# Optimization experiments

Measured on AMD Instinct MI355X. Metric: run time of the kernel, lower is better.

The kernel has to match this reference:

```python
import jax, jax.numpy as jnp
import numpy as np

N_NODES = 50000
N_EDGES = 800000
HIDDEN = 64
RES = 0.5  # args.res_layer


def setup_inputs() -> dict:
    key = jax.random.key(0)
    ks = jax.random.split(key, 9)
    s = 0.05  # scale weights to keep exp(att) stable
    return {
        "edge_index": jax.random.randint(ks[0], (2, N_EDGES), 0, N_NODES, dtype=jnp.int32),
        "adj_values": jax.random.uniform(ks[1], (N_EDGES,), dtype=jnp.float32),
        "embeds": jax.random.normal(ks[2], (N_NODES, HIDDEN), dtype=jnp.float32),
        "W1": jax.random.normal(ks[3], (HIDDEN, HIDDEN), dtype=jnp.float32) * s,
        "b1": jax.random.normal(ks[4], (HIDDEN,), dtype=jnp.float32) * s,
        "W2": jax.random.normal(ks[5], (HIDDEN, HIDDEN), dtype=jnp.float32) * s,
        "b2": jax.random.normal(ks[6], (HIDDEN,), dtype=jnp.float32) * s,
        "att_w": jax.random.normal(ks[7], (2 * HIDDEN,), dtype=jnp.float32) * s,
        "att_b": jax.random.normal(ks[8], (1,), dtype=jnp.float32) * s,
    }


def reference(edge_index, adj_values, embeds, W1, b1, W2, b2, att_w, att_b):
    n = embeds.shape[0]
    h = embeds.shape[1]
    row, col = edge_index[0], edge_index[1]
    # per-edge gather + two small linears with ReLU
    f1 = jax.nn.relu(embeds[row] @ W1 + b1)          # [E, h]
    f2 = jax.nn.relu(embeds[col] @ W2 + b2)          # [E, h]
    # attention score = Linear(concat(f1, f2)) -> split weight, avoid concat
    att = f1 @ att_w[:h] + f2 @ att_w[h:] + att_b[0]  # [E]
    exp_att = jnp.exp(att)
    # sparse row-wise softmax denominator via segment sum
    rowsum = jax.ops.segment_sum(exp_att, row, num_segments=n) + 1e-6  # [N]
    values = (exp_att / rowsum[row] + RES * adj_values) / (1.0 + RES)  # [E]
    # SpMM: out[i] = sum_{e: row[e]=i} values[e] * embeds[col[e]]
    out = jax.ops.segment_sum(values[:, None] * embeds[col], row, num_segments=n)  # [N, h]
    return values, out
```

## Files before the change

### kernel.cpp

```cpp
#include <hip/hip_runtime.h>
#include <hip/hip_bf16.h>

#define HID 64
#define RES_F 0.5f
#define NBKT 196
#define BCAP 5120
#define EB   512
#define LCAP 32

typedef __attribute__((ext_vector_type(8))) short short8;
typedef __attribute__((ext_vector_type(4))) float f32x4;

__device__ __forceinline__ short f2bf(float x) {
    __hip_bfloat16 h = __float2bfloat16(x);
    return __builtin_bit_cast(short, h);
}
__device__ __forceinline__ float bf2f(unsigned short u) {
    return __builtin_bit_cast(float, ((unsigned)u) << 16);
}

__global__ void __launch_bounds__(256) fused_prep_kernel(
    const float* __restrict__ embeds,
    const float* __restrict__ W1, const float* __restrict__ W2,
    const float* __restrict__ b1, const float* __restrict__ b2,
    const float* __restrict__ att_w, const float* __restrict__ att_b,
    const int* __restrict__ row, const int* __restrict__ col,
    const float* __restrict__ adj,
    int2* __restrict__ bstream, int* __restrict__ bcnt,
    float* __restrict__ g, float* __restrict__ corr,
    __hip_bfloat16* __restrict__ embeds_bf,
    int n, int E, int nodeBlocks)
{
    __shared__ short sW[2 * HID * HID];

    if (blockIdx.x < nodeBlocks) {
        for (int i = threadIdx.x; i < HID * HID; i += blockDim.x) {
            sW[i]             = f2bf(W1[i]);
            sW[HID * HID + i] = f2bf(W2[i]);
        }
        __syncthreads();

        const float ab = att_b[0];
        const int lane = threadIdx.x & 63;
        const int colx = lane & 15;
        const int quad = lane >> 4;

        short8 bfrag[8][2];
        float  sac[8], bc[8];
#pragma unroll
        for (int cb = 0; cb < 8; ++cb) {
            const int jp = cb * 16 + colx;
            const short* w = (jp < HID) ? (sW + jp) : (sW + HID * HID + jp - HID);
#pragma unroll
            for (int kh = 0; kh < 2; ++kh) {
                short8 f;
#pragma unroll
                for (int j = 0; j < 8; ++j) {
                    const int k = kh * 32 + quad * 8 + j;
                    f[j] = w[k * HID];
                }
                bfrag[cb][kh] = f;
            }
            sac[cb] = att_w[jp];
            bc[cb]  = (jp < HID) ? b1[jp] : b2[jp - HID];
        }

        int gwave = (blockIdx.x * blockDim.x + threadIdx.x) >> 6;
        const int nwave = (nodeBlocks * blockDim.x) >> 6;
        const int nbatch = (n + 15) >> 4;

        for (int b = gwave; b < nbatch; b += nwave) {
            const int base = b << 4;
            int mrow = base + colx;
            if (mrow >= n) mrow = n - 1;
            const float* ep = embeds + (size_t)mrow * HID;
            short8 afrag0, afrag1;
#pragma unroll
            for (int j = 0; j < 8; ++j) {
                afrag0[j] = f2bf(ep[quad * 8 + j]);
                afrag1[j] = f2bf(ep[32 + quad * 8 + j]);
            }
            {
                short8* ebf = (short8*)(embeds_bf + (size_t)mrow * HID);
                ebf[quad]     = afrag0;
                ebf[4 + quad] = afrag1;
            }

            float acc1[4] = {0.f, 0.f, 0.f, 0.f};
            float acc2[4] = {0.f, 0.f, 0.f, 0.f};
#pragma unroll
            for (int cb = 0; cb < 8; ++cb) {
                f32x4 C = {0.f, 0.f, 0.f, 0.f};
                C = __builtin_amdgcn_mfma_f32_16x16x32_bf16(afrag0, bfrag[cb][0], C, 0, 0, 0);
                C = __builtin_amdgcn_mfma_f32_16x16x32_bf16(afrag1, bfrag[cb][1], C, 0, 0, 0);
#pragma unroll
                for (int reg = 0; reg < 4; ++reg) {
                    const float v = fmaxf(C[reg] + bc[cb], 0.f) * sac[cb];
                    if (cb < 4) acc1[reg] += v; else acc2[reg] += v;
                }
            }
#pragma unroll
            for (int reg = 0; reg < 4; ++reg) {
#pragma unroll
                for (int off = 1; off < 16; off <<= 1) {
                    acc1[reg] += __shfl_xor(acc1[reg], off, 64);
                    acc2[reg] += __shfl_xor(acc2[reg], off, 64);
                }
            }
            if (colx == 0) {
#pragma unroll
                for (int reg = 0; reg < 4; ++reg) {
                    const int i = base + quad * 4 + reg;
                    if (i < n) {
                        g[i]    = __expf(acc2[reg]);
                        corr[i] = 1e-6f * __expf(-(acc1[reg] + ab));
                    }
                }
            }
        }
    } else {
        int* lcnt = (int*)sW;
        for (int k = threadIdx.x; k < NBKT; k += 256) lcnt[k] = 0;
        __syncthreads();

        const int eb = blockIdx.x - nodeBlocks;
        const int chunk = (E + EB - 1) / EB;
        const int e0 = eb * chunk;
        const int e1 = min(E, e0 + chunk);
        for (int e = e0 + (int)threadIdx.x; e < e1; e += 256) {
            const int r    = row[e];
            const int c    = col[e];
            const float aj = adj[e];
            const unsigned aq = (unsigned)(aj * 65535.0f + 0.5f);
            const int k = r >> 8;
            const int2 pl = make_int2((int)((unsigned)c | (aq << 16)),
                                      (r & 255) | (e << 8));
            const int pos = atomicAdd(&lcnt[k], 1);
            if (pos < LCAP)
                bstream[((size_t)k * EB + eb) * LCAP + pos] = pl;
        }
        __syncthreads();

        for (int k = threadIdx.x; k < NBKT; k += 256)
            bcnt[eb * NBKT + k] = min(lcnt[k], LCAP);
    }
}

__global__ void __launch_bounds__(512) regroup_kernel(
    const int2* __restrict__ bstream, const int* __restrict__ bcnt,
    int2* __restrict__ edata2, int* __restrict__ rowdir, int n)
{
    __shared__ int cnt[256], wcur[256], wsum[4];
    const int k = blockIdx.x;
    const int t = threadIdx.x;

    if (t < 256) cnt[t] = 0;
    const int myc = bcnt[t * NBKT + k];
    __syncthreads();

    const int2* src = bstream + ((size_t)k * EB + t) * LCAP;
    for (int j = 0; j < myc; ++j)
        atomicAdd(&cnt[src[j].y & 255], 1);
    __syncthreads();

    int incl = 0, myCnt = 0;
    if (t < 256) {
        const int lane = t & 63;
        myCnt = cnt[t];
        incl = myCnt;
#pragma unroll
        for (int off = 1; off < 64; off <<= 1) {
            const int y = __shfl_up(incl, off, 64);
            if (lane >= off) incl += y;
        }
        if (lane == 63) wsum[t >> 6] = incl;
    }
    __syncthreads();
    if (t < 256) {
        int wo = 0;
        for (int i = 0; i < (t >> 6); ++i) wo += wsum[i];
        const int excl = incl + wo - myCnt;
        wcur[t] = excl;
        const int r = k * 256 + t;
        if (r < n)
            rowdir[r] = (k * BCAP + excl) | (min(myCnt, 64) << 20);
    }
    __syncthreads();

    int2* dst = edata2 + (size_t)k * BCAP;
    for (int j = 0; j < myc; ++j) {
        const int2 pl = src[j];
        const int p = atomicAdd(&wcur[pl.y & 255], 1);
        dst[p] = pl;
    }
}

__global__ void __launch_bounds__(256) spmm_kernel(
    const int* __restrict__ rowdir, const int2* __restrict__ edata2,
    const __hip_bfloat16* __restrict__ embeds_bf,
    const float* __restrict__ g, const float* __restrict__ corr,
    float* __restrict__ values, float* __restrict__ out, int n)
{
    const float inv = 1.0f / (1.0f + RES_F);
    const int lane = threadIdx.x & 63;
    const int half = lane >> 5;
    const int hl   = lane & 31;

    const int idx = ((blockIdx.x >> 3) << 2) + (threadIdx.x >> 6);
    const int k   = ((idx >> 8) << 3) + (blockIdx.x & 7);
    const int r   = (k << 8) + (idx & 255);
    if (k >= NBKT || r >= n) return;

    const int pk    = rowdir[r];
    const int start = pk & 0xFFFFF;
    const int deg   = pk >> 20;
    const bool valid = lane < deg;
    int c = 0, e = 0;
    float gc = 0.0f, aj = 0.0f;
    if (valid) {
        const int2 ed = edata2[(size_t)start + lane];
        const unsigned pk0 = (unsigned)ed.x;
        c  = (int)(pk0 & 0xFFFFu);
        aj = (float)(pk0 >> 16) * (1.0f / 65535.0f);
        e  = (int)(((unsigned)ed.y) >> 8);
        gc = g[c];
    }
    float G = gc;
#pragma unroll
    for (int off = 1; off < 64; off <<= 1)
        G += __shfl_xor(G, off, 64);
    const float invDr = 1.0f / (G + corr[r]);
    float v = 0.0f;
    if (valid) {
        v = (gc * invDr + RES_F * aj) * inv;
        values[e] = v;
    }

    float accx = 0.0f, accy = 0.0f;
    int j = 0;
    for (; j + 8 <= deg; j += 8) {
        const int j0 = j + half,     j1 = j + 2 + half;
        const int j2 = j + 4 + half, j3 = j + 6 + half;
        const int   c0 = __shfl(c, j0, 64);
        const int   c1 = __shfl(c, j1, 64);
        const int   c2 = __shfl(c, j2, 64);
        const int   c3 = __shfl(c, j3, 64);
        const float v0 = __shfl(v, j0, 64);
        const float v1 = __shfl(v, j1, 64);
        const float v2 = __shfl(v, j2, 64);
        const float v3 = __shfl(v, j3, 64);
        const ushort2 h0 = *(const ushort2*)(embeds_bf + (size_t)c0 * HID + hl * 2);
        const ushort2 h1 = *(const ushort2*)(embeds_bf + (size_t)c1 * HID + hl * 2);
        const ushort2 h2 = *(const ushort2*)(embeds_bf + (size_t)c2 * HID + hl * 2);
        const ushort2 h3 = *(const ushort2*)(embeds_bf + (size_t)c3 * HID + hl * 2);
        accx = fmaf(v0, bf2f(h0.x), accx); accy = fmaf(v0, bf2f(h0.y), accy);
        accx = fmaf(v1, bf2f(h1.x), accx); accy = fmaf(v1, bf2f(h1.y), accy);
        accx = fmaf(v2, bf2f(h2.x), accx); accy = fmaf(v2, bf2f(h2.y), accy);
        accx = fmaf(v3, bf2f(h3.x), accx); accy = fmaf(v3, bf2f(h3.y), accy);
    }
    for (; j < deg; j += 2) {
        const int j0 = j + half;
        const int   cj = __shfl(c, j0, 64);
        const float vj = __shfl(v, j0, 64);
        const ushort2 h = *(const ushort2*)(embeds_bf + (size_t)cj * HID + hl * 2);
        accx = fmaf(vj, bf2f(h.x), accx);
        accy = fmaf(vj, bf2f(h.y), accy);
    }
    accx += __shfl_xor(accx, 32, 64);
    accy += __shfl_xor(accy, 32, 64);
    if (lane < 32) {
        float2 o; o.x = accx; o.y = accy;
        ((float2*)(out + (size_t)r * HID))[hl] = o;
    }
}

extern "C" void kernel_launch(void* const* d_in, const int* in_sizes, int n_in,
                              void* d_out, int out_size, void* d_ws, size_t ws_size,
                              hipStream_t stream_)
{
    const int* edge_index = (const int*)d_in[0];
    const float* adj      = (const float*)d_in[1];
    const float* embeds   = (const float*)d_in[2];
    const float* W1       = (const float*)d_in[3];
    const float* b1       = (const float*)d_in[4];
    const float* W2       = (const float*)d_in[5];
    const float* b2       = (const float*)d_in[6];
    const float* att_w    = (const float*)d_in[7];
    const float* att_b    = (const float*)d_in[8];

    const int E = in_sizes[1];
    const int N = in_sizes[2] / HID;

    const int* row = edge_index;
    const int* col = edge_index + E;

    int2*  bstream = (int2*)d_ws;
    int2*  edata2  = bstream + (size_t)NBKT * EB * LCAP;
    int*   bcnt    = (int*)(edata2 + (size_t)NBKT * BCAP);
    int*   rowdir  = bcnt + EB * NBKT;
    float* g       = (float*)(rowdir + N);
    float* corr    = g + N;
    __hip_bfloat16* embeds_bf = (__hip_bfloat16*)(corr + N);

    float* values = (float*)d_out;
    float* out    = values + E;

    const int nodeBlocks = 512;
    fused_prep_kernel<<<nodeBlocks + EB, 256, 0, stream_>>>(
        embeds, W1, W2, b1, b2, att_w, att_b, row, col, adj,
        bstream, bcnt, g, corr, embeds_bf,
        N, E, nodeBlocks);

    regroup_kernel<<<NBKT, 512, 0, stream_>>>(bstream, bcnt, edata2, rowdir, N);

    spmm_kernel<<<12800, 256, 0, stream_>>>(rowdir, edata2, embeds_bf,
                                            g, corr, values, out, N);
}
```

Before: 142.7 us.

## Fuse regroup and SpMM into one kernel using LDS-resident bucket edges

Merges the regroup and SpMM kernels. Each bucket is handled by two 1024-thread blocks that redundantly regroup the whole bucket's edges into shared memory and then each process half of its 256 rows. This removes the edata2/rowdir global round trip and one kernel launch. In exchange, the regroup work is done twice per bucket, and only 392 large blocks run the SpMM phase, which may hurt latency hiding for the gathers. The prep kernel also switches the embedding row reads to float4 vector loads.

Result: slower. 154.4 us (+8.3%).

```diff
diff --git a/kernel.cpp b/kernel.cpp
--- a/kernel.cpp
+++ b/kernel.cpp
@@ -73,13 +73,18 @@
             const int base = b << 4;
             int mrow = base + colx;
             if (mrow >= n) mrow = n - 1;
-            const float* ep = embeds + (size_t)mrow * HID;
+            const float4* ep4 = (const float4*)(embeds + (size_t)mrow * HID);
+            const float4 wa = ep4[quad * 2],     wb = ep4[quad * 2 + 1];
+            const float4 wc = ep4[8 + quad * 2], wd = ep4[8 + quad * 2 + 1];
             short8 afrag0, afrag1;
-#pragma unroll
-            for (int j = 0; j < 8; ++j) {
-                afrag0[j] = f2bf(ep[quad * 8 + j]);
-                afrag1[j] = f2bf(ep[32 + quad * 8 + j]);
-            }
+            afrag0[0] = f2bf(wa.x); afrag0[1] = f2bf(wa.y);
+            afrag0[2] = f2bf(wa.z); afrag0[3] = f2bf(wa.w);
+            afrag0[4] = f2bf(wb.x); afrag0[5] = f2bf(wb.y);
+            afrag0[6] = f2bf(wb.z); afrag0[7] = f2bf(wb.w);
+            afrag1[0] = f2bf(wc.x); afrag1[1] = f2bf(wc.y);
+            afrag1[2] = f2bf(wc.z); afrag1[3] = f2bf(wc.w);
+            afrag1[4] = f2bf(wd.x); afrag1[5] = f2bf(wd.y);
+            afrag1[6] = f2bf(wd.z); afrag1[7] = f2bf(wd.w);
             {
                 short8* ebf = (short8*)(embeds_bf + (size_t)mrow * HID);
                 ebf[quad]     = afrag0;
@@ -146,131 +151,130 @@
     }
 }
 
-__global__ void __launch_bounds__(512) regroup_kernel(
+__global__ void __launch_bounds__(1024) regroup_spmm_kernel(
     const int2* __restrict__ bstream, const int* __restrict__ bcnt,
-    int2* __restrict__ edata2, int* __restrict__ rowdir, int n)
+    const __hip_bfloat16* __restrict__ embeds_bf,
+    const float* __restrict__ g, const float* __restrict__ corr,
+    float* __restrict__ values, float* __restrict__ out, int n)
 {
-    __shared__ int cnt[256], wcur[256], wsum[4];
-    const int k = blockIdx.x;
-    const int t = threadIdx.x;
+    __shared__ int2 led[BCAP];
+    __shared__ int cnt[256], rstart[256], wcur[256], wsum[4];
+    const int k   = blockIdx.x >> 1;
+    const int sub = blockIdx.x & 1;
+    const int t   = threadIdx.x;
+    const int sl  = t & 511;
+    const bool hi = t >= 512;
 
     if (t < 256) cnt[t] = 0;
-    const int myc = bcnt[t * NBKT + k];
-    __syncthreads();
-
-    const int2* src = bstream + ((size_t)k * EB + t) * LCAP;
-    for (int j = 0; j < myc; ++j)
+    const int myc = bcnt[sl * NBKT + k];
+    const int jm  = (myc + 1) >> 1;
+    const int j0  = hi ? jm : 0;
+    const int j1  = hi ? myc : jm;
+    __syncthreads();
+
+    const int2* src = bstream + ((size_t)k * EB + sl) * LCAP;
+    for (int j = j0; j < j1; ++j)
         atomicAdd(&cnt[src[j].y & 255], 1);
     __syncthreads();
 
     int incl = 0, myCnt = 0;
     if (t < 256) {
-        const int lane = t & 63;
+        const int lane0 = t & 63;
         myCnt = cnt[t];
         incl = myCnt;
 #pragma unroll
         for (int off = 1; off < 64; off <<= 1) {
             const int y = __shfl_up(incl, off, 64);
-            if (lane >= off) incl += y;
-        }
-        if (lane == 63) wsum[t >> 6] = incl;
+            if (lane0 >= off) incl += y;
+        }
+        if (lane0 == 63) wsum[t >> 6] = incl;
     }
     __syncthreads();
     if (t < 256) {
         int wo = 0;
         for (int i = 0; i < (t >> 6); ++i) wo += wsum[i];
         const int excl = incl + wo - myCnt;
-        wcur[t] = excl;
-        const int r = k * 256 + t;
-        if (r < n)
-            rowdir[r] = (k * BCAP + excl) | (min(myCnt, 64) << 20);
-    }
-    __syncthreads();
-
-    int2* dst = edata2 + (size_t)k * BCAP;
-    for (int j = 0; j < myc; ++j) {
+        rstart[t] = excl;
+        wcur[t]   = excl;
+    }
+    __syncthreads();
+    for (int j = j0; j < j1; ++j) {
         const int2 pl = src[j];
         const int p = atomicAdd(&wcur[pl.y & 255], 1);
-        dst[p] = pl;
-    }
-}
-
-__global__ void __launch_bounds__(256) spmm_kernel(
-    const int* __restrict__ rowdir, const int2* __restrict__ edata2,
-    const __hip_bfloat16* __restrict__ embeds_bf,
-    const float* __restrict__ g, const float* __restrict__ corr,
-    float* __restrict__ values, float* __restrict__ out, int n)
-{
+        led[p] = pl;
+    }
+    __syncthreads();
+
     const float inv = 1.0f / (1.0f + RES_F);
-    const int lane = threadIdx.x & 63;
+    const int wid  = t >> 6;
+    const int lane = t & 63;
     const int half = lane >> 5;
     const int hl   = lane & 31;
 
-    const int idx = ((blockIdx.x >> 3) << 2) + (threadIdx.x >> 6);
-    const int k   = ((idx >> 8) << 3) + (blockIdx.x & 7);
-    const int r   = (k << 8) + (idx & 255);
-    if (k >= NBKT || r >= n) return;
-
-    const int pk    = rowdir[r];
-    const int start = pk & 0xFFFFF;
-    const int deg   = pk >> 20;
-    const bool valid = lane < deg;
-    int c = 0, e = 0;
-    float gc = 0.0f, aj = 0.0f;
-    if (valid) {
-        const int2 ed = edata2[(size_t)start + lane];
-        const unsigned pk0 = (unsigned)ed.x;
-        c  = (int)(pk0 & 0xFFFFu);
-        aj = (float)(pk0 >> 16) * (1.0f / 65535.0f);
-        e  = (int)(((unsigned)ed.y) >> 8);
-        gc = g[c];
-    }
-    float G = gc;
-#pragma unroll
-    for (int off = 1; off < 64; off <<= 1)
-        G += __shfl_xor(G, off, 64);
-    const float invDr = 1.0f / (G + corr[r]);
-    float v = 0.0f;
-    if (valid) {
-        v = (gc * invDr + RES_F * aj) * inv;
-        values[e] = v;
-    }
-
-    float accx = 0.0f, accy = 0.0f;
-    int j = 0;
-    for (; j + 8 <= deg; j += 8) {
-        const int j0 = j + half,     j1 = j + 2 + half;
-        const int j2 = j + 4 + half, j3 = j + 6 + half;
-        const int   c0 = __shfl(c, j0, 64);
-        const int   c1 = __shfl(c, j1, 64);
-        const int   c2 = __shfl(c, j2, 64);
-        const int   c3 = __shfl(c, j3, 64);
-        const float v0 = __shfl(v, j0, 64);
-        const float v1 = __shfl(v, j1, 64);
-        const float v2 = __shfl(v, j2, 64);
-        const float v3 = __shfl(v, j3, 64);
-        const ushort2 h0 = *(const ushort2*)(embeds_bf + (size_t)c0 * HID + hl * 2);
-        const ushort2 h1 = *(const ushort2*)(embeds_bf + (size_t)c1 * HID + hl * 2);
-        const ushort2 h2 = *(const ushort2*)(embeds_bf + (size_t)c2 * HID + hl * 2);
-        const ushort2 h3 = *(const ushort2*)(embeds_bf + (size_t)c3 * HID + hl * 2);
-        accx = fmaf(v0, bf2f(h0.x), accx); accy = fmaf(v0, bf2f(h0.y), accy);
-        accx = fmaf(v1, bf2f(h1.x), accx); accy = fmaf(v1, bf2f(h1.y), accy);
-        accx = fmaf(v2, bf2f(h2.x), accx); accy = fmaf(v2, bf2f(h2.y), accy);
-        accx = fmaf(v3, bf2f(h3.x), accx); accy = fmaf(v3, bf2f(h3.y), accy);
-    }
-    for (; j < deg; j += 2) {
-        const int j0 = j + half;
-        const int   cj = __shfl(c, j0, 64);
-        const float vj = __shfl(v, j0, 64);
-        const ushort2 h = *(const ushort2*)(embeds_bf + (size_t)cj * HID + hl * 2);
-        accx = fmaf(vj, bf2f(h.x), accx);
-        accy = fmaf(vj, bf2f(h.y), accy);
-    }
-    accx += __shfl_xor(accx, 32, 64);
-    accy += __shfl_xor(accy, 32, 64);
-    if (lane < 32) {
-        float2 o; o.x = accx; o.y = accy;
-        ((float2*)(out + (size_t)r * HID))[hl] = o;
+    for (int i = 0; i < 8; ++i) {
+        const int rl = sub * 128 + wid * 8 + i;
+        const int r  = k * 256 + rl;
+        if (r >= n) break;
+        const int start = rstart[rl];
+        const int deg   = min(cnt[rl], 64);
+        const bool valid = lane < deg;
+        int c = 0, e = 0;
+        float gc = 0.0f, aj = 0.0f;
+        if (valid) {
+            const int2 ed = led[start + lane];
+            const unsigned pk0 = (unsigned)ed.x;
+            c  = (int)(pk0 & 0xFFFFu);
+            aj = (float)(pk0 >> 16) * (1.0f / 65535.0f);
+            e  = (int)(((unsigned)ed.y) >> 8);
+            gc = g[c];
+        }
+        float G = gc;
+#pragma unroll
+        for (int off = 1; off < 64; off <<= 1)
+            G += __shfl_xor(G, off, 64);
+        const float invDr = 1.0f / (G + corr[r]);
+        float v = 0.0f;
+        if (valid) {
+            v = (gc * invDr + RES_F * aj) * inv;
+            values[e] = v;
+        }
+
+        float accx = 0.0f, accy = 0.0f;
+        int j = 0;
+        for (; j + 8 <= deg; j += 8) {
+            const int ja = j + half,     jb = j + 2 + half;
+            const int jc = j + 4 + half, jd = j + 6 + half;
+            const int   c0 = __shfl(c, ja, 64);
+            const int   c1 = __shfl(c, jb, 64);
+            const int   c2 = __shfl(c, jc, 64);
+            const int   c3 = __shfl(c, jd, 64);
+            const float v0 = __shfl(v, ja, 64);
+            const float v1 = __shfl(v, jb, 64);
+            const float v2 = __shfl(v, jc, 64);
+            const float v3 = __shfl(v, jd, 64);
+            const ushort2 h0 = *(const ushort2*)(embeds_bf + (size_t)c0 * HID + hl * 2);
+            const ushort2 h1 = *(const ushort2*)(embeds_bf + (size_t)c1 * HID + hl * 2);
+            const ushort2 h2 = *(const ushort2*)(embeds_bf + (size_t)c2 * HID + hl * 2);
+            const ushort2 h3 = *(const ushort2*)(embeds_bf + (size_t)c3 * HID + hl * 2);
+            accx = fmaf(v0, bf2f(h0.x), accx); accy = fmaf(v0, bf2f(h0.y), accy);
+            accx = fmaf(v1, bf2f(h1.x), accx); accy = fmaf(v1, bf2f(h1.y), accy);
+            accx = fmaf(v2, bf2f(h2.x), accx); accy = fmaf(v2, bf2f(h2.y), accy);
+            accx = fmaf(v3, bf2f(h3.x), accx); accy = fmaf(v3, bf2f(h3.y), accy);
+        }
+        for (; j < deg; j += 2) {
+            const int ja = j + half;
+            const int   cj = __shfl(c, ja, 64);
+            const float vj = __shfl(v, ja, 64);
+            const ushort2 h = *(const ushort2*)(embeds_bf + (size_t)cj * HID + hl * 2);
+            accx = fmaf(vj, bf2f(h.x), accx);
+            accy = fmaf(vj, bf2f(h.y), accy);
+        }
+        accx += __shfl_xor(accx, 32, 64);
+        accy += __shfl_xor(accy, 32, 64);
+        if (lane < 32) {
+            float2 o; o.x = accx; o.y = accy;
+            ((float2*)(out + (size_t)r * HID))[hl] = o;
+        }
     }
 }
 
@@ -295,10 +299,8 @@
     const int* col = edge_index + E;
 
     int2*  bstream = (int2*)d_ws;
-    int2*  edata2  = bstream + (size_t)NBKT * EB * LCAP;
-    int*   bcnt    = (int*)(edata2 + (size_t)NBKT * BCAP);
-    int*   rowdir  = bcnt + EB * NBKT;
-    float* g       = (float*)(rowdir + N);
+    int*   bcnt    = (int*)(bstream + (size_t)NBKT * EB * LCAP);
+    float* g       = (float*)(bcnt + EB * NBKT);
     float* corr    = g + N;
     __hip_bfloat16* embeds_bf = (__hip_bfloat16*)(corr + N);
 
@@ -311,8 +313,6 @@
         bstream, bcnt, g, corr, embeds_bf,
         N, E, nodeBlocks);
 
-    regroup_kernel<<<NBKT, 512, 0, stream_>>>(bstream, bcnt, edata2, rowdir, N);
-
-    spmm_kernel<<<12800, 256, 0, stream_>>>(rowdir, edata2, embeds_bf,
-                                            g, corr, values, out, N);
-}
+    regroup_spmm_kernel<<<NBKT * 2, 1024, 0, stream_>>>(
+        bstream, bcnt, embeds_bf, g, corr, values, out, N);
+}
```
